# Optimization experiments

Measured on AMD Instinct MI355X. Metric: run time of the kernel, lower is better.

## Reference

```python
import jax, jax.numpy as jnp
import numpy as np

EPS = 1e-5            # BatchNorm3d eps (running_mean=0, running_var=1 at init)
SCALE = 0.025         # patchmatch_interval_scale
NEIGHBORS = 9         # evaluate_neighbors
PROP_OUT = 1          # propagation_out_range - 1


def conv1x1(x, w):
    # 1x1x1 Conv3d, no bias: x [B,C,D,H,W], w [O,C]
    return jnp.einsum('bcdhw,oc->bodhw', x, w)


def conv_bn_relu(x, w, g, b):
    # ConvBnReLU3D with BN at init stats (mean 0, var 1)
    y = conv1x1(x, w)
    y = g[None, :, None, None, None] * y / jnp.sqrt(1.0 + EPS) + b[None, :, None, None, None]
    return jax.nn.relu(y)


def neighbor_gather_sum(x, offset):
    # x [B,D,H,W]; offset [B,2*NEIGHBORS,H,W]
    # Reflection-pad then take 9 statically-offset windows at two dilations,
    # weight each by per-pixel offsets, and average the two scales.
    B, D, H, W = x.shape
    side = int(np.sqrt(NEIGHBORS))                 # 3
    p1 = side // 2 + PROP_OUT                      # 2
    p2 = p1 * 2                                    # 4
    X1 = jnp.pad(x, ((0, 0), (0, 0), (p1, p1), (p1, p1)), mode='reflect')
    X2 = jnp.pad(x, ((0, 0), (0, 0), (p2, p2), (p2, p2)), mode='reflect')
    acc = jnp.zeros_like(x)
    for s in range(NEIGHBORS):
        iy = (s // side) * (PROP_OUT + 1)
        ix = (s % side) * (PROP_OUT + 1)
        f1 = offset[:, s, None] * X2[:, :, 2 * iy:2 * iy + H, 2 * ix:2 * ix + W]
        f = offset[:, s + NEIGHBORS, None] * X1[:, :, iy:iy + H, ix:ix + W]
        acc = acc + (f + f1) * 0.5
    return acc


def setup_inputs():
    key = jax.random.key(0)
    ks = jax.random.split(key, 10)
    B, G, D, H, W = 2, 8, 16, 256, 320
    x1 = jax.random.normal(ks[0], (B, G, D, H, W), jnp.float32)
    offset = jax.random.uniform(ks[1], (B, 2 * NEIGHBORS, H, W), jnp.float32)
    depth_min = jnp.full((B,), 425.0, jnp.float32)
    depth_max = jnp.full((B,), 935.0, jnp.float32)
    depth_sample = 425.0 + 510.0 * jax.random.uniform(ks[2], (B, D, H, W), jnp.float32)
    w = lambda k, s: 0.1 * jax.random.normal(k, s, jnp.float32)
    return dict(
        x1=x1, offset=offset, depth_sample=depth_sample,
        depth_min=depth_min, depth_max=depth_max,
        s_w0=w(ks[3], (16, G)), s_g0=jnp.ones((16,)), s_b0=jnp.zeros((16,)),
        s_w1=w(ks[4], (8, 16)), s_g1=jnp.ones((8,)), s_b1=jnp.zeros((8,)),
        s_w2=w(ks[5], (1, 8)), s_bias2=jnp.zeros((1,)),
        p_w0=w(ks[6], (16, G)), p_g0=jnp.ones((16,)), p_b0=jnp.zeros((16,)),
        p_w1=w(ks[7], (8, 16)), p_g1=jnp.ones((8,)), p_b1=jnp.zeros((8,)),
        p_w2=w(ks[8], (1, 8)), p_bias2=jnp.zeros((1,)),
    )


def reference(x1, offset, depth_sample, depth_min, depth_max,
              s_w0, s_g0, s_b0, s_w1, s_g1, s_b1, s_w2, s_bias2,
              p_w0, p_g0, p_b0, p_w1, p_g1, p_b1, p_w2, p_bias2):
    # --- PixelwiseNet: per-pixel view weight from the group cost volume ---
    h = conv_bn_relu(x1, p_w0, p_g0, p_b0)
    h = conv_bn_relu(h, p_w1, p_g1, p_b1)
    h = conv1x1(h, p_w2) + p_bias2[None, :, None, None, None]
    vw = jax.nn.sigmoid(h[:, 0])                   # [B,D,H,W]
    view_weight = jnp.max(vw, axis=1, keepdims=True)  # [B,1,H,W]

    # --- Depth_weight: adaptive neighbor depth-similarity weight ---
    inv_min = 1.0 / depth_min
    inv_max = 1.0 / depth_max
    xn = (1.0 / depth_sample - inv_max[:, None, None, None]) / \
         (inv_min - inv_max)[:, None, None, None]  # normalized inverse depth
    xg = neighbor_gather_sum(xn, offset)
    dw = jax.nn.sigmoid((2.0 - jnp.clip(jnp.abs(xg - xn) / SCALE, 0.0, 4.0)) * 2.0)

    # --- SimilarityNet on view-weighted cost volume ---
    x1w = x1 * view_weight[:, None]                # [B,G,D,H,W]
    s = conv_bn_relu(x1w, s_w0, s_g0, s_b0)
    s = conv_bn_relu(s, s_w1, s_g1, s_b1)
    s = (conv1x1(s, s_w2) + s_bias2[None, :, None, None, None])[:, 0]  # [B,D,H,W]
    score = neighbor_gather_sum(s, offset) * dw

    attn = jax.nn.softmax(score, axis=1)
    depth = jnp.sum(depth_sample * attn, axis=1)   # [B,H,W]
    return depth
```

## Files before the change

kernel.cpp:

```cpp
#include <hip/hip_runtime.h>
#include <math.h>

constexpr int B = 2, G = 8, D = 16, H = 256, W = 320;
constexpr int HW = H * W;
constexpr float EPS = 1e-5f;
constexpr int WSTRIDE = 320;

typedef _Float16 h2 __attribute__((ext_vector_type(2)));

#if __has_builtin(__builtin_amdgcn_fdot2)
#define FDOT2(a, b, c) __builtin_amdgcn_fdot2((a), (b), (c), false)
#else
#define FDOT2(a, b, c) fmaf((float)(a).x, (float)(b).x, fmaf((float)(a).y, (float)(b).y, (c)))
#endif

__device__ __forceinline__ float sigmoidf_(float x) {
    return 1.0f / (1.0f + __expf(-x));
}

__device__ __forceinline__ int reflect_(int i, int n) {
    return i < 0 ? -i : (i >= n ? 2 * n - 2 - i : i);
}

__device__ __forceinline__ void pack_net_(
    const float* __restrict__ w0, const float* __restrict__ g0, const float* __restrict__ b0,
    const float* __restrict__ w1, const float* __restrict__ g1, const float* __restrict__ b1,
    const float* __restrict__ w2, const float* __restrict__ bias2,
    float* __restrict__ o, int t, float rs)
{
    if (t < 64) {
        const int oo = t >> 2, j = t & 3;
        const float s = g0[oo] * rs;
        h2 v; v.x = (_Float16)(w0[oo * 8 + 2 * j] * s);
        v.y = (_Float16)(w0[oo * 8 + 2 * j + 1] * s);
        ((h2*)o)[t] = v;
    } else if (t < 128) {
        const int u = t - 64, oo = u >> 3, j = u & 7;
        const float s = g1[oo] * rs;
        h2 v; v.x = (_Float16)(w1[oo * 16 + 2 * j] * s);
        v.y = (_Float16)(w1[oo * 16 + 2 * j + 1] * s);
        ((h2*)o)[t] = v;
    } else if (t < 132) {
        const int u = t - 128;
        h2 v; v.x = (_Float16)w2[2 * u];
        v.y = (_Float16)w2[2 * u + 1];
        ((h2*)o)[t] = v;
    } else if (t < 148) {
        o[t] = b0[t - 132];
    } else if (t < 156) {
        o[t] = b1[t - 148];
    } else if (t == 156) {
        o[t] = bias2[0];
    }
}

__global__ __launch_bounds__(256) void k_prep(
    const float* __restrict__ sw0, const float* __restrict__ sg0, const float* __restrict__ sb0,
    const float* __restrict__ sw1, const float* __restrict__ sg1, const float* __restrict__ sb1,
    const float* __restrict__ sw2, const float* __restrict__ sbias2,
    const float* __restrict__ pw0, const float* __restrict__ pg0, const float* __restrict__ pb0,
    const float* __restrict__ pw1, const float* __restrict__ pg1, const float* __restrict__ pb1,
    const float* __restrict__ pw2, const float* __restrict__ pbias2,
    float* __restrict__ wbuf)
{
    const int t = threadIdx.x;
    const float rs = rsqrtf(1.0f + EPS);
    pack_net_(pw0, pg0, pb0, pw1, pg1, pb1, pw2, pbias2, wbuf, t, rs);
    pack_net_(sw0, sg0, sb0, sw1, sg1, sb1, sw2, sbias2, wbuf + WSTRIDE, t, rs);
}

__device__ __forceinline__ float mlph_(const float* __restrict__ Wb, const h2 xh[4])
{
    const h2* __restrict__ W0 = (const h2*)Wb;
    const h2* __restrict__ W1 = (const h2*)Wb + 64;
    const h2* __restrict__ W2 = (const h2*)Wb + 128;
    const float* __restrict__ B0 = Wb + 132;
    const float* __restrict__ B1 = Wb + 148;

    float l1[16];
    #pragma unroll
    for (int o = 0; o < 16; ++o) {
        float a = B0[o];
        #pragma unroll
        for (int j = 0; j < 4; ++j) a = FDOT2(W0[o * 4 + j], xh[j], a);
        l1[o] = fmaxf(a, 0.0f);
    }
    h2 l1h[8];
    #pragma unroll
    for (int j = 0; j < 8; ++j) {
        h2 v; v.x = (_Float16)l1[2 * j]; v.y = (_Float16)l1[2 * j + 1];
        l1h[j] = v;
    }
    float l2[8];
    #pragma unroll
    for (int o = 0; o < 8; ++o) {
        float a = B1[o];
        #pragma unroll
        for (int j = 0; j < 8; ++j) a = FDOT2(W1[o * 8 + j], l1h[j], a);
        l2[o] = fmaxf(a, 0.0f);
    }
    h2 l2h[4];
    #pragma unroll
    for (int j = 0; j < 4; ++j) {
        h2 v; v.x = (_Float16)l2[2 * j]; v.y = (_Float16)l2[2 * j + 1];
        l2h[j] = v;
    }
    float h = Wb[156];
    #pragma unroll
    for (int j = 0; j < 4; ++j) h = FDOT2(W2[j], l2h[j], h);
    return h;
}

__global__ __launch_bounds__(1024, 8) void k_fused(
    const float* __restrict__ x1,
    const float* __restrict__ depth_sample,
    const float* __restrict__ depth_min, const float* __restrict__ depth_max,
    const float* __restrict__ wP, const float* __restrict__ wS,
    float* __restrict__ s_out, float* __restrict__ xn_out)
{
    __shared__ float red[16][64];

    const int tid = threadIdx.x;
    const int pi = tid & 63;
    const int dt = tid >> 6;
    const int pid = blockIdx.x * 64 + pi;
    const int b = pid / HW;
    const int p = pid - b * HW;

    const float* xp = x1 + ((size_t)(b * G * D) + dt) * HW + p;
    float x[8];
    #pragma unroll
    for (int g = 0; g < 8; ++g) x[g] = xp[(size_t)g * D * HW];
    h2 xh[4];
    #pragma unroll
    for (int j = 0; j < 4; ++j) {
        h2 v; v.x = (_Float16)x[2 * j]; v.y = (_Float16)x[2 * j + 1];
        xh[j] = v;
    }

    red[dt][pi] = mlph_(wP, xh);
    __syncthreads();

    float mx = red[0][pi];
    #pragma unroll
    for (int k = 1; k < 16; ++k) mx = fmaxf(mx, red[k][pi]);
    const float vw = sigmoidf_(mx);

    h2 vwh; vwh.x = (_Float16)vw; vwh.y = (_Float16)vw;
    h2 xsh[4];
    #pragma unroll
    for (int j = 0; j < 4; ++j) xsh[j] = xh[j] * vwh;
    const float hS = mlph_(wS, xsh);

    const size_t oidx = (size_t)(b * D + dt) * HW + p;
    s_out[oidx] = hS;

    const float inv_min = 1.0f / depth_min[b];
    const float inv_max = 1.0f / depth_max[b];
    const float rinv = 1.0f / (inv_min - inv_max);
    const float ds = depth_sample[oidx];
    xn_out[oidx] = (1.0f / ds - inv_max) * rinv;
}

__global__ __launch_bounds__(1024, 8) void k_score_depth(
    const float* __restrict__ s_arr, const float* __restrict__ xn,
    const float* __restrict__ offset, const float* __restrict__ depth_sample,
    float* __restrict__ out)
{
    __shared__ float off_lds[18][64];
    __shared__ float redM[16][64];
    __shared__ float redS[16][64];
    __shared__ float redA[16][64];

    const int bid = blockIdx.x;
    const int wg = (bid & 7) * 320 + (bid >> 3);

    const int tid = threadIdx.x;
    const int pi = tid & 63;
    const int dt = tid >> 6;
    const int pg0_ = wg * 64;
    const int b = pg0_ / HW;
    const int pb0 = pg0_ - b * HW;
    const int p = pb0 + pi;
    const int h = p / W;
    const int w = p - h * W;

    const float* ob = offset + (size_t)b * 18 * HW + pb0;
    for (int idx = tid; idx < 18 * 64; idx += 1024) {
        const int s = idx >> 6, qq = idx & 63;
        off_lds[s][qq] = ob[(size_t)s * HW + qq];
    }
    __syncthreads();

    int a1s[9], a2s[9];
    {
        int ry1[3], ry2[3], cx1[3], cx2[3];
        #pragma unroll
        for (int i = 0; i < 3; ++i) {
            ry1[i] = reflect_(h + (i - 1) * 2, H) * W;
            ry2[i] = reflect_(h + (i - 1) * 4, H) * W;
            cx1[i] = reflect_(w + (i - 1) * 2, W);
            cx2[i] = reflect_(w + (i - 1) * 4, W);
        }
        #pragma unroll
        for (int s = 0; s < 9; ++s) {
            a1s[s] = ry1[s / 3] + cx1[s % 3];
            a2s[s] = ry2[s / 3] + cx2[s % 3];
        }
    }

    const size_t bbase = (size_t)b * D * HW;
    const float* sd = s_arr + bbase + (size_t)dt * HW;
    const float* xd = xn + bbase + (size_t)dt * HW;

    float accs = 0.0f, accx = 0.0f;
    #pragma unroll
    for (int s = 0; s < 9; ++s) {
        const float w1 = off_lds[s + 9][pi];
        const float w2 = off_lds[s][pi];
        accs += 0.5f * (w1 * sd[a1s[s]] + w2 * sd[a2s[s]]);
        accx += 0.5f * (w1 * xd[a1s[s]] + w2 * xd[a2s[s]]);
    }
    const float xc = xd[p];
    const float diff = fminf(fabsf(accx - xc) * 40.0f, 4.0f);
    const float dwv = sigmoidf_((2.0f - diff) * 2.0f);
    const float score = accs * dwv;
    const float dsv = depth_sample[bbase + (size_t)dt * HW + p];

    redM[dt][pi] = score;
    __syncthreads();
    float m = redM[0][pi];
    #pragma unroll
    for (int k = 1; k < 16; ++k) m = fmaxf(m, redM[k][pi]);

    const float e = __expf(score - m);
    redS[dt][pi] = e;
    redA[dt][pi] = dsv * e;
    __syncthreads();

    if (dt == 0) {
        float sum = 0.0f, acc = 0.0f;
        #pragma unroll
        for (int k = 0; k < 16; ++k) { sum += redS[k][pi]; acc += redA[k][pi]; }
        out[pg0_ + pi] = acc / sum;
    }
}

extern "C" void kernel_launch(void* const* d_in, const int* in_sizes, int n_in,
                              void* d_out, int out_size, void* d_ws, size_t ws_size,
                              hipStream_t stream)
{
    const float* x1           = (const float*)d_in[0];
    const float* offset       = (const float*)d_in[1];
    const float* depth_sample = (const float*)d_in[2];
    const float* depth_min    = (const float*)d_in[3];
    const float* depth_max    = (const float*)d_in[4];
    const float* s_w0 = (const float*)d_in[5];
    const float* s_g0 = (const float*)d_in[6];
    const float* s_b0 = (const float*)d_in[7];
    const float* s_w1 = (const float*)d_in[8];
    const float* s_g1 = (const float*)d_in[9];
    const float* s_b1 = (const float*)d_in[10];
    const float* s_w2 = (const float*)d_in[11];
    const float* s_bias2 = (const float*)d_in[12];
    const float* p_w0 = (const float*)d_in[13];
    const float* p_g0 = (const float*)d_in[14];
    const float* p_b0 = (const float*)d_in[15];
    const float* p_w1 = (const float*)d_in[16];
    const float* p_g1 = (const float*)d_in[17];
    const float* p_b1 = (const float*)d_in[18];
    const float* p_w2 = (const float*)d_in[19];
    const float* p_bias2 = (const float*)d_in[20];

    float* s_arr = (float*)d_ws;
    float* xn    = s_arr + (size_t)B * D * HW;
    float* wbuf  = xn + (size_t)B * D * HW;

    k_prep<<<1, 256, 0, stream>>>(
        s_w0, s_g0, s_b0, s_w1, s_g1, s_b1, s_w2, s_bias2,
        p_w0, p_g0, p_b0, p_w1, p_g1, p_b1, p_w2, p_bias2, wbuf);

    k_fused<<<(B * HW) / 64, 1024, 0, stream>>>(
        x1, depth_sample, depth_min, depth_max,
        wbuf, wbuf + WSTRIDE, s_arr, xn);

    k_score_depth<<<(B * HW) / 64, 1024, 0, stream>>>(
        s_arr, xn, offset, depth_sample, (float*)d_out);
}
```

Before: 71.84 us.

## Process four pixels per thread in score kernel and pack MLP activations

The score/depth kernel now gives each thread four adjacent pixels and uses float4 loads for the neighbor windows, with a scalar reflect fallback only at row edges, cutting block size from 1024 to 256 threads. This is meant to reduce per-element address arithmetic and the number of memory instructions in the gather-heavy stage. The MLP also packs activations with cvt_pkrtz and applies a packed half max for the ReLU, which skips the fp32 intermediate arrays. The risks are round-toward-zero conversion changing precision slightly, unaligned float2 loads at odd offsets, and fewer threads available to hide latency.

```diff
diff --git a/kernel.cpp b/kernel.cpp
--- a/kernel.cpp
+++ b/kernel.cpp
@@ -7,6 +7,7 @@
 constexpr int WSTRIDE = 320;
 
 typedef _Float16 h2 __attribute__((ext_vector_type(2)));
+typedef float f4v __attribute__((ext_vector_type(4)));
 
 #if __has_builtin(__builtin_amdgcn_fdot2)
 #define FDOT2(a, b, c) __builtin_amdgcn_fdot2((a), (b), (c), false)
@@ -14,12 +15,26 @@
 #define FDOT2(a, b, c) fmaf((float)(a).x, (float)(b).x, fmaf((float)(a).y, (float)(b).y, (c)))
 #endif
 
+static __device__ __forceinline__ h2 cvtpk_(float a, float b) {
+#if __has_builtin(__builtin_amdgcn_cvt_pkrtz)
+    return __builtin_bit_cast(h2, __builtin_amdgcn_cvt_pkrtz(a, b));
+#else
+    h2 v; v.x = (_Float16)a; v.y = (_Float16)b; return v;
+#endif
+}
+
 __device__ __forceinline__ float sigmoidf_(float x) {
     return 1.0f / (1.0f + __expf(-x));
 }
 
 __device__ __forceinline__ int reflect_(int i, int n) {
     return i < 0 ? -i : (i >= n ? 2 * n - 2 - i : i);
+}
+
+__device__ __forceinline__ f4v ld4u_(const float* p) {
+    const float2 a = *reinterpret_cast<const float2*>(p);
+    const float2 b = *reinterpret_cast<const float2*>(p + 2);
+    f4v r; r.x = a.x; r.y = a.y; r.z = b.x; r.w = b.y; return r;
 }
 
 __device__ __forceinline__ void pack_net_(
@@ -76,34 +91,29 @@
     const h2* __restrict__ W2 = (const h2*)Wb + 128;
     const float* __restrict__ B0 = Wb + 132;
     const float* __restrict__ B1 = Wb + 148;
-
-    float l1[16];
-    #pragma unroll
-    for (int o = 0; o < 16; ++o) {
-        float a = B0[o];
-        #pragma unroll
-        for (int j = 0; j < 4; ++j) a = FDOT2(W0[o * 4 + j], xh[j], a);
-        l1[o] = fmaxf(a, 0.0f);
-    }
+    const h2 zz = {};
+
     h2 l1h[8];
     #pragma unroll
-    for (int j = 0; j < 8; ++j) {
-        h2 v; v.x = (_Float16)l1[2 * j]; v.y = (_Float16)l1[2 * j + 1];
-        l1h[j] = v;
-    }
-    float l2[8];
-    #pragma unroll
     for (int o = 0; o < 8; ++o) {
-        float a = B1[o];
-        #pragma unroll
-        for (int j = 0; j < 8; ++j) a = FDOT2(W1[o * 8 + j], l1h[j], a);
-        l2[o] = fmaxf(a, 0.0f);
+        float a0 = B0[2 * o], a1 = B0[2 * o + 1];
+        #pragma unroll
+        for (int j = 0; j < 4; ++j) {
+            a0 = FDOT2(W0[(2 * o) * 4 + j], xh[j], a0);
+            a1 = FDOT2(W0[(2 * o + 1) * 4 + j], xh[j], a1);
+        }
+        l1h[o] = __builtin_elementwise_max(cvtpk_(a0, a1), zz);
     }
     h2 l2h[4];
     #pragma unroll
-    for (int j = 0; j < 4; ++j) {
-        h2 v; v.x = (_Float16)l2[2 * j]; v.y = (_Float16)l2[2 * j + 1];
-        l2h[j] = v;
+    for (int o = 0; o < 4; ++o) {
+        float a0 = B1[2 * o], a1 = B1[2 * o + 1];
+        #pragma unroll
+        for (int j = 0; j < 8; ++j) {
+            a0 = FDOT2(W1[(2 * o) * 8 + j], l1h[j], a0);
+            a1 = FDOT2(W1[(2 * o + 1) * 8 + j], l1h[j], a1);
+        }
+        l2h[o] = __builtin_elementwise_max(cvtpk_(a0, a1), zz);
     }
     float h = Wb[156];
     #pragma unroll
@@ -133,10 +143,7 @@
     for (int g = 0; g < 8; ++g) x[g] = xp[(size_t)g * D * HW];
     h2 xh[4];
     #pragma unroll
-    for (int j = 0; j < 4; ++j) {
-        h2 v; v.x = (_Float16)x[2 * j]; v.y = (_Float16)x[2 * j + 1];
-        xh[j] = v;
-    }
+    for (int j = 0; j < 4; ++j) xh[j] = cvtpk_(x[2 * j], x[2 * j + 1]);
 
     red[dt][pi] = mlph_(wP, xh);
     __syncthreads();
@@ -162,87 +169,118 @@
     xn_out[oidx] = (1.0f / ds - inv_max) * rinv;
 }
 
-__global__ __launch_bounds__(1024, 8) void k_score_depth(
+__global__ __launch_bounds__(256, 8) void k_score_depth(
     const float* __restrict__ s_arr, const float* __restrict__ xn,
     const float* __restrict__ offset, const float* __restrict__ depth_sample,
     float* __restrict__ out)
 {
     __shared__ float off_lds[18][64];
-    __shared__ float redM[16][64];
-    __shared__ float redS[16][64];
-    __shared__ float redA[16][64];
+    __shared__ f4v redM[16][16];
+    __shared__ f4v redS[16][16];
+    __shared__ f4v redA[16][16];
 
     const int bid = blockIdx.x;
     const int wg = (bid & 7) * 320 + (bid >> 3);
 
     const int tid = threadIdx.x;
-    const int pi = tid & 63;
-    const int dt = tid >> 6;
+    const int q = tid & 15;
+    const int dt = tid >> 4;
     const int pg0_ = wg * 64;
     const int b = pg0_ / HW;
     const int pb0 = pg0_ - b * HW;
-    const int p = pb0 + pi;
-    const int h = p / W;
-    const int w = p - h * W;
+    const int p4 = pb0 + 4 * q;
+    const int h = p4 / W;
+    const int w0 = p4 - h * W;
 
     const float* ob = offset + (size_t)b * 18 * HW + pb0;
-    for (int idx = tid; idx < 18 * 64; idx += 1024) {
+    for (int idx = tid; idx < 18 * 64; idx += 256) {
         const int s = idx >> 6, qq = idx & 63;
         off_lds[s][qq] = ob[(size_t)s * HW + qq];
     }
     __syncthreads();
 
-    int a1s[9], a2s[9];
-    {
-        int ry1[3], ry2[3], cx1[3], cx2[3];
-        #pragma unroll
-        for (int i = 0; i < 3; ++i) {
-            ry1[i] = reflect_(h + (i - 1) * 2, H) * W;
-            ry2[i] = reflect_(h + (i - 1) * 4, H) * W;
-            cx1[i] = reflect_(w + (i - 1) * 2, W);
-            cx2[i] = reflect_(w + (i - 1) * 4, W);
-        }
-        #pragma unroll
-        for (int s = 0; s < 9; ++s) {
-            a1s[s] = ry1[s / 3] + cx1[s % 3];
-            a2s[s] = ry2[s / 3] + cx2[s % 3];
-        }
+    int ry1[3], ry2[3];
+    #pragma unroll
+    for (int i = 0; i < 3; ++i) {
+        ry1[i] = reflect_(h + (i - 1) * 2, H) * W;
+        ry2[i] = reflect_(h + (i - 1) * 4, H) * W;
     }
 
     const size_t bbase = (size_t)b * D * HW;
     const float* sd = s_arr + bbase + (size_t)dt * HW;
     const float* xd = xn + bbase + (size_t)dt * HW;
 
-    float accs = 0.0f, accx = 0.0f;
-    #pragma unroll
-    for (int s = 0; s < 9; ++s) {
-        const float w1 = off_lds[s + 9][pi];
-        const float w2 = off_lds[s][pi];
-        accs += 0.5f * (w1 * sd[a1s[s]] + w2 * sd[a2s[s]]);
-        accx += 0.5f * (w1 * xd[a1s[s]] + w2 * xd[a2s[s]]);
-    }
-    const float xc = xd[p];
-    const float diff = fminf(fabsf(accx - xc) * 40.0f, 4.0f);
-    const float dwv = sigmoidf_((2.0f - diff) * 2.0f);
-    const float score = accs * dwv;
-    const float dsv = depth_sample[bbase + (size_t)dt * HW + p];
-
-    redM[dt][pi] = score;
+    f4v accs = {}, accx = {};
+    const bool edge = (w0 == 0) || (w0 == W - 4);
+    if (!edge) {
+        #pragma unroll
+        for (int s = 0; s < 9; ++s) {
+            const int sy = s / 3, sx = s % 3;
+            const int dx1 = (sx - 1) * 2, dx2 = (sx - 1) * 4;
+            const f4v w1 = *(const f4v*)&off_lds[s + 9][4 * q];
+            const f4v w2 = *(const f4v*)&off_lds[s][4 * q];
+            const int a1 = ry1[sy] + w0 + dx1;
+            const int a2 = ry2[sy] + w0 + dx2;
+            const f4v t1 = (dx1 & 3) ? ld4u_(sd + a1) : *(const f4v*)(sd + a1);
+            const f4v t2 = *(const f4v*)(sd + a2);
+            const f4v u1 = (dx1 & 3) ? ld4u_(xd + a1) : *(const f4v*)(xd + a1);
+            const f4v u2 = *(const f4v*)(xd + a2);
+            accs += 0.5f * (w1 * t1 + w2 * t2);
+            accx += 0.5f * (w1 * u1 + w2 * u2);
+        }
+    } else {
+        #pragma unroll
+        for (int px = 0; px < 4; ++px) {
+            const int w = w0 + px;
+            int cx1[3], cx2[3];
+            #pragma unroll
+            for (int i = 0; i < 3; ++i) {
+                cx1[i] = reflect_(w + (i - 1) * 2, W);
+                cx2[i] = reflect_(w + (i - 1) * 4, W);
+            }
+            float as = 0.0f, ax = 0.0f;
+            #pragma unroll
+            for (int s = 0; s < 9; ++s) {
+                const int sy = s / 3, sx = s % 3;
+                const float w1 = off_lds[s + 9][4 * q + px];
+                const float w2 = off_lds[s][4 * q + px];
+                const int a1 = ry1[sy] + cx1[sx];
+                const int a2 = ry2[sy] + cx2[sx];
+                as += 0.5f * (w1 * sd[a1] + w2 * sd[a2]);
+                ax += 0.5f * (w1 * xd[a1] + w2 * xd[a2]);
+            }
+            accs[px] = as; accx[px] = ax;
+        }
+    }
+
+    const f4v xc = *(const f4v*)(xd + p4);
+    f4v score;
+    #pragma unroll
+    for (int px = 0; px < 4; ++px) {
+        const float diff = fminf(fabsf(accx[px] - xc[px]) * 40.0f, 4.0f);
+        const float dwv = sigmoidf_((2.0f - diff) * 2.0f);
+        score[px] = accs[px] * dwv;
+    }
+    const f4v dsv = *(const f4v*)(depth_sample + bbase + (size_t)dt * HW + p4);
+
+    redM[dt][q] = score;
     __syncthreads();
-    float m = redM[0][pi];
-    #pragma unroll
-    for (int k = 1; k < 16; ++k) m = fmaxf(m, redM[k][pi]);
-
-    const float e = __expf(score - m);
-    redS[dt][pi] = e;
-    redA[dt][pi] = dsv * e;
+    f4v m = redM[0][q];
+    #pragma unroll
+    for (int k = 1; k < 16; ++k) m = __builtin_elementwise_max(m, redM[k][q]);
+
+    f4v e;
+    #pragma unroll
+    for (int px = 0; px < 4; ++px) e[px] = __expf(score[px] - m[px]);
+    redS[dt][q] = e;
+    redA[dt][q] = dsv * e;
     __syncthreads();
 
     if (dt == 0) {
-        float sum = 0.0f, acc = 0.0f;
-        #pragma unroll
-        for (int k = 0; k < 16; ++k) { sum += redS[k][pi]; acc += redA[k][pi]; }
-        out[pg0_ + pi] = acc / sum;
+        f4v sum = {}, acc = {};
+        #pragma unroll
+        for (int k = 0; k < 16; ++k) { sum += redS[k][q]; acc += redA[k][q]; }
+        *(f4v*)(out + pg0_ + 4 * q) = acc / sum;
     }
 }
 
@@ -284,6 +322,6 @@
         x1, depth_sample, depth_min, depth_max,
         wbuf, wbuf + WSTRIDE, s_arr, xn);
 
-    k_score_depth<<<(B * HW) / 64, 1024, 0, stream>>>(
+    k_score_depth<<<(B * HW) / 64, 256, 0, stream>>>(
         s_arr, xn, offset, depth_sample, (float*)d_out);
 }
```

After: 132.4 us. 84.3% more time.
